# Kernel tuning notes

Hardware: AMD Instinct MI355X
Metric: run time of the kernel (lower is better)

Reference implementation:

```python
import jax, jax.numpy as jnp
import numpy as np

B, S, D, J, NI = 8192, 20, 300, 512, 1000
VG = 2048 + 5 * 6  # vis_dim + 5*6 = guide feature dim


def setup_inputs() -> dict:
    key = jax.random.key(0)
    ks = jax.random.split(key, 11)
    context = jax.random.normal(ks[0], (B, S, D), jnp.float32)
    embedded = jax.random.normal(ks[1], (B, S, D), jnp.float32)
    input_labels = jax.random.randint(ks[2], (B, S), 0, 10000, dtype=jnp.int64)
    # guarantee at least one valid token per row (avoid divide-by-zero renorm)
    input_labels = input_labels.at[:, 0].set(jnp.maximum(input_labels[:, 0], 1))
    guide_input = jax.random.normal(ks[3], (NI, VG), jnp.float32)
    sent_to_image_ann = jax.random.randint(ks[4], (2 * B,), 0, NI, dtype=jnp.int64)
    # parameters (PyTorch Linear: y = x @ W.T + b)
    W_sent = jax.random.normal(ks[5], (J, D), jnp.float32) * 0.02
    b_sent = jnp.zeros((J,), jnp.float32)
    W_emb = jax.random.normal(ks[6], (J, VG), jnp.float32) * 0.02
    b_emb = jnp.zeros((J,), jnp.float32)
    w_fc = jax.random.normal(ks[7], (J,), jnp.float32) * 0.02
    b_fc = jnp.zeros((), jnp.float32)
    return {"context": context, "embedded": embedded, "input_labels": input_labels,
            "guide_input": guide_input, "sent_to_image_ann": sent_to_image_ann,
            "W_sent": W_sent, "b_sent": b_sent, "W_emb": W_emb, "b_emb": b_emb,
            "w_fc": w_fc, "b_fc": b_fc}


def reference(context, embedded, input_labels, guide_input, sent_to_image_ann,
              W_sent, b_sent, W_emb, b_emb, w_fc, b_fc):
    # prefix-valid mask: loop in original breaks at first zero label
    nonzero = (input_labels != 0).astype(jnp.float32)          # (B,S)
    valid = jnp.cumprod(nonzero, axis=1)                        # (B,S)
    # per-sentence guide feature: guide_input[sent_to_image_ann[2*i]]
    fea = guide_input[sent_to_image_ann[::2]]                   # (B,VG)
    # fc_embed(guidance): guidance rows are fea (valid prefix) or 0 (else),
    # so the linear output is fea@W_emb.T+b_emb or just b_emb.
    fea_emb = fea @ W_emb.T + b_emb                             # (B,J)
    guid_emb = valid[:, :, None] * fea_emb[:, None, :] + (1.0 - valid)[:, :, None] * b_emb
    cxt_emb = jnp.einsum('bsd,jd->bsj', context, W_sent) + b_sent
    H = jnp.tanh(cxt_emb + guid_emb)                            # (B,S,J)
    scores = jnp.einsum('bsj,j->bs', H, w_fc) + b_fc            # (B,S)
    attn = jax.nn.softmax(scores, axis=1)
    attn = attn * nonzero
    attn = attn / jnp.sum(attn, axis=1, keepdims=True)
    weighted_cxt = jnp.einsum('bs,bsd->bd', attn, embedded)     # (B,D)
    return weighted_cxt
```

## Files before the change

kernel.cpp:

```cpp
#include <hip/hip_runtime.h>
#include <hip/hip_bf16.h>

#define BB 8192
#define SS 20
#define DD 300
#define JJ 512
#define NII 1000
#define VGG 2078
#define BP1 72

typedef __attribute__((ext_vector_type(8))) short short8v;
typedef __attribute__((ext_vector_type(4))) float float4v;

__device__ __forceinline__ unsigned short bf16u(float x) {
    __hip_bfloat16 h = __float2bfloat16(x);
    return *(unsigned short*)&h;
}

__global__ __launch_bounds__(256) void kc_pad2(const float* __restrict__ W_emb,
                                               const float* __restrict__ guide,
                                               __hip_bfloat16* __restrict__ Web,
                                               __hip_bfloat16* __restrict__ Gb) {
    long idx = (long)blockIdx.x * 256 + threadIdx.x;
    if (idx >= 1512L * 2112) return;
    int r = (int)(idx / 2112), c = (int)(idx % 2112);
    if (r < JJ) {
        float v = (c < VGG) ? W_emb[(long)r * VGG + c] : 0.f;
        Web[(long)r * 2112 + c] = __float2bfloat16(v);
    } else {
        int g = r - JJ;
        float v = (c < VGG) ? guide[(long)g * VGG + c] : 0.f;
        Gb[(long)g * 2112 + c] = __float2bfloat16(v);
    }
}

__global__ __launch_bounds__(256) void kc_prep_wt(const float* __restrict__ W_sent,
                                                  const float* __restrict__ b_sent,
                                                  const float* __restrict__ b_emb,
                                                  __hip_bfloat16* __restrict__ dst) {
    int idx = blockIdx.x * 256 + threadIdx.x;
    if (idx >= 40 * 512) return;
    int kb = idx >> 9, col = idx & 511;
#pragma unroll
    for (int e = 0; e < 8; ++e) {
        int k = kb * 8 + e;
        float v = (k < DD) ? W_sent[(long)col * DD + k]
                : (k == DD) ? b_sent[col]
                : (k == DD + 1) ? b_emb[col] : 0.f;
        dst[(long)idx * 8 + e] = __float2bfloat16(v);
    }
}

__global__ __launch_bounds__(512) void kS_sumwf(const float* __restrict__ w_fc,
                                                float* __restrict__ out) {
    __shared__ float part[8];
    int t = threadIdx.x;
    float v = w_fc[t];
    v += __shfl_xor(v, 1);  v += __shfl_xor(v, 2);  v += __shfl_xor(v, 4);
    v += __shfl_xor(v, 8);  v += __shfl_xor(v, 16); v += __shfl_xor(v, 32);
    if ((t & 63) == 0) part[t >> 6] = v;
    __syncthreads();
    if (t == 0) {
        float s = 0.f;
#pragma unroll
        for (int i = 0; i < 8; ++i) s += part[i];
        out[0] = s;
    }
}

__global__ __launch_bounds__(256) void k0_valid(const int* __restrict__ labels,
                                                float* __restrict__ valid,
                                                float* __restrict__ nonzero) {
    int b = blockIdx.x * blockDim.x + threadIdx.x;
    if (b >= BB) return;
    float v = 1.f;
    for (int s = 0; s < SS; ++s) {
        float nz = (labels[b * SS + s] != 0) ? 1.f : 0.f;
        v *= nz;
        nonzero[b * SS + s] = nz;
        valid[b * SS + s] = v;
    }
}

__global__ __launch_bounds__(256) void k1_femb_mfma(
    const __hip_bfloat16* __restrict__ Gb,
    const __hip_bfloat16* __restrict__ Web,
    const float* __restrict__ b_emb,
    __hip_bfloat16* __restrict__ femb) {
    __shared__ __hip_bfloat16 Al[64 * BP1];
    __shared__ __hip_bfloat16 Bl[64 * BP1];
    const int t = threadIdx.x;
    const int m0 = blockIdx.x * 64;
    const int n0 = blockIdx.y * 64;
    const int lane = t & 63;
    const int w = t >> 6;
    const int wm = w >> 1, wn = w & 1;
    const int li = lane & 15, lq = lane >> 4;

    float4v acc[2][2] = {};

    for (int kt = 0; kt < 33; ++kt) {
        for (int c = t; c < 512; c += 256) {
            int rr = c >> 3, off = (c & 7) * 8;
            int gr = m0 + rr; if (gr > NII - 1) gr = NII - 1;
            *(uint4*)&Al[rr * BP1 + off] =
                *(const uint4*)(Gb + (long)gr * 2112 + kt * 64 + off);
            *(uint4*)&Bl[rr * BP1 + off] =
                *(const uint4*)(Web + (long)(n0 + rr) * 2112 + kt * 64 + off);
        }
        __syncthreads();
#pragma unroll
        for (int ks = 0; ks < 2; ++ks) {
            short8v a[2], b[2];
#pragma unroll
            for (int mt = 0; mt < 2; ++mt)
                a[mt] = *(const short8v*)&Al[(wm * 32 + mt * 16 + li) * BP1 + ks * 32 + lq * 8];
#pragma unroll
            for (int nt = 0; nt < 2; ++nt)
                b[nt] = *(const short8v*)&Bl[(wn * 32 + nt * 16 + li) * BP1 + ks * 32 + lq * 8];
#pragma unroll
            for (int mt = 0; mt < 2; ++mt)
#pragma unroll
                for (int nt = 0; nt < 2; ++nt)
                    acc[mt][nt] = __builtin_amdgcn_mfma_f32_16x16x32_bf16(
                        a[mt], b[nt], acc[mt][nt], 0, 0, 0);
        }
        __syncthreads();
    }
#pragma unroll
    for (int nt = 0; nt < 2; ++nt) {
        int col = n0 + wn * 32 + nt * 16 + li;
        float be = b_emb[col];
#pragma unroll
        for (int mt = 0; mt < 2; ++mt)
#pragma unroll
            for (int reg = 0; reg < 4; ++reg) {
                int row = wm * 32 + mt * 16 + lq * 4 + reg;
                femb[(long)(m0 + row) * JJ + col] = __float2bfloat16(acc[mt][nt][reg] + be);
            }
    }
}

__global__ __launch_bounds__(256)
__attribute__((amdgpu_waves_per_eu(2, 4)))
void k2_scores_mfma(
    const float* __restrict__ context,
    const __hip_bfloat16* __restrict__ Wt,
    const float* __restrict__ w_fc,
    const float* __restrict__ b_fc,
    const float* __restrict__ sumwf,
    const __hip_bfloat16* __restrict__ femb,
    const int* __restrict__ ann,
    const float* __restrict__ valid,
    float* __restrict__ scores) {
    const int t = threadIdx.x;
    const int wid = t >> 6, lane = t & 63;
    const int li = lane & 15, lq = lane >> 4;
    const int m0 = blockIdx.x * 64 + wid * 16;

    const float* crow = context + (long)(m0 + li) * DD;
    const float vA = valid[m0 + li];
    short8v areg[10];
#pragma unroll
    for (int kt = 0; kt < 9; ++kt) {
        const int k0 = kt * 32 + lq * 8;
        float4 u = *(const float4*)(crow + k0);
        float4 v2 = *(const float4*)(crow + k0 + 4);
        short8v a;
        a[0] = (short)bf16u(u.x);  a[1] = (short)bf16u(u.y);
        a[2] = (short)bf16u(u.z);  a[3] = (short)bf16u(u.w);
        a[4] = (short)bf16u(v2.x); a[5] = (short)bf16u(v2.y);
        a[6] = (short)bf16u(v2.z); a[7] = (short)bf16u(v2.w);
        areg[kt] = a;
    }
    {
        short8v a = {0, 0, 0, 0, 0, 0, 0, 0};
        if (lq == 0) {
            float4 u = *(const float4*)(crow + 288);
            float4 v2 = *(const float4*)(crow + 292);
            a[0] = (short)bf16u(u.x);  a[1] = (short)bf16u(u.y);
            a[2] = (short)bf16u(u.z);  a[3] = (short)bf16u(u.w);
            a[4] = (short)bf16u(v2.x); a[5] = (short)bf16u(v2.y);
            a[6] = (short)bf16u(v2.z); a[7] = (short)bf16u(v2.w);
        } else if (lq == 1) {
            float4 u = *(const float4*)(crow + 296);
            a[0] = (short)bf16u(u.x);  a[1] = (short)bf16u(u.y);
            a[2] = (short)bf16u(u.z);  a[3] = (short)bf16u(u.w);
            a[4] = (short)bf16u(1.f);  a[5] = (short)bf16u(1.f - vA);
        }
        areg[9] = a;
    }

    const int mslot = m0 + lq * 4;
    const int b0r = mslot / SS;
    const int b3r = (mslot + 3) / SS;
    const int g0 = ann[2 * b0r];
    const int g1 = ann[2 * b3r];
    float vmc[4]; unsigned selm[4];
#pragma unroll
    for (int reg = 0; reg < 4; ++reg) {
        vmc[reg] = valid[mslot + reg];
        selm[reg] = (((mslot + reg) / SS) != b0r) ? 0xffffffffu : 0u;
    }
    const unsigned short* fp = (const unsigned short*)femb;
    const __hip_bfloat16* pb = Wt + ((long)lq * 512 + li) * 8;

    float sp[4] = {0.f, 0.f, 0.f, 0.f};

    auto loadB = [&](short8v (&buf)[20], int np) {
        const __hip_bfloat16* pn = pb + (long)np * 256;
#pragma unroll
        for (int kt = 0; kt < 10; ++kt) {
            buf[2 * kt]     = *(const short8v*)(pn + (long)kt * 16384);
            buf[2 * kt + 1] = *(const short8v*)(pn + (long)kt * 16384 + 128);
        }
    };
    auto computeB = [&](short8v (&buf)[20], int np) {
        const int colA = np * 32 + li;
        const int colB = colA + 16;
        const unsigned uA = ((unsigned)fp[(long)g1 * JJ + colA] << 16) | fp[(long)g0 * JJ + colA];
        const unsigned uB = ((unsigned)fp[(long)g1 * JJ + colB] << 16) | fp[(long)g0 * JJ + colB];
        const float wfA = w_fc[colA];
        const float wfB = w_fc[colB];
        float4v a0 = {0.f, 0.f, 0.f, 0.f}, a1 = {0.f, 0.f, 0.f, 0.f};
#pragma unroll
        for (int kt = 0; kt < 10; ++kt) {
            a0 = __builtin_amdgcn_mfma_f32_16x16x32_bf16(areg[kt], buf[2 * kt], a0, 0, 0, 0);
            a1 = __builtin_amdgcn_mfma_f32_16x16x32_bf16(areg[kt], buf[2 * kt + 1], a1, 0, 0, 0);
        }
        const unsigned floA = uA << 16, fhiA = uA & 0xffff0000u;
        const unsigned floB = uB << 16, fhiB = uB & 0xffff0000u;
#pragma unroll
        for (int reg = 0; reg < 4; ++reg) {
            const float fvA = __uint_as_float((floA & ~selm[reg]) | (fhiA & selm[reg]));
            const float xA = fmaf(vmc[reg], fvA, a0[reg]);
            const float eA = __expf(xA + xA);
            sp[reg] = fmaf(wfA, __builtin_amdgcn_rcpf(eA + 1.f), sp[reg]);
            const float fvB = __uint_as_float((floB & ~selm[reg]) | (fhiB & selm[reg]));
            const float xB = fmaf(vmc[reg], fvB, a1[reg]);
            const float eB = __expf(xB + xB);
            sp[reg] = fmaf(wfB, __builtin_amdgcn_rcpf(eB + 1.f), sp[reg]);
        }
    };

    short8v bufA[20], bufB[20];
    loadB(bufA, 0);
    for (int nq = 0; nq < 8; ++nq) {
        const int npA = nq * 2;
        loadB(bufB, npA + 1);
        computeB(bufA, npA);
        if (npA + 2 < 16) loadB(bufA, npA + 2);
        computeB(bufB, npA + 1);
    }

    const float base = b_fc[0] + sumwf[0];
#pragma unroll
    for (int reg = 0; reg < 4; ++reg) {
        float v = sp[reg];
        v += __shfl_xor(v, 1); v += __shfl_xor(v, 2);
        v += __shfl_xor(v, 4); v += __shfl_xor(v, 8);
        if (li == 0) scores[mslot + reg] = base - 2.f * v;
    }
}

__global__ __launch_bounds__(256) void k3_out(const float* __restrict__ scores,
                                              const float* __restrict__ nonzero,
                                              const float* __restrict__ embedded,
                                              float* __restrict__ out) {
    __shared__ float wgt[3][SS];
    const int b0 = blockIdx.x * 3;
    const int t = threadIdx.x;
    if (t < 3) {
        int b = b0 + t;
        if (b < BB) {
            float sc[SS], nz[SS];
            float mx = -1e30f;
            for (int s = 0; s < SS; ++s) {
                sc[s] = scores[b * SS + s];
                nz[s] = nonzero[b * SS + s];
                mx = fmaxf(mx, sc[s]);
            }
            float den = 0.f, e[SS];
            for (int s = 0; s < SS; ++s) { e[s] = nz[s] * __expf(sc[s] - mx); den += e[s]; }
            float inv = 1.f / den;
            for (int s = 0; s < SS; ++s) wgt[t][s] = e[s] * inv;
        }
    }
    __syncthreads();
    if (t < 225) {
        int r = t / 75, q = t - r * 75;
        int b = b0 + r;
        if (b < BB) {
            float4 a; a.x = a.y = a.z = a.w = 0.f;
#pragma unroll
            for (int s = 0; s < SS; ++s) {
                float4 e = *(const float4*)(embedded + ((long)b * SS + s) * DD + q * 4);
                float ww = wgt[r][s];
                a.x += ww * e.x; a.y += ww * e.y; a.z += ww * e.z; a.w += ww * e.w;
            }
            *(float4*)(out + (long)b * DD + q * 4) = a;
        }
    }
}

extern "C" void kernel_launch(void* const* d_in, const int* in_sizes, int n_in,
                              void* d_out, int out_size, void* d_ws, size_t ws_size,
                              hipStream_t stream) {
    const float* context  = (const float*)d_in[0];
    const float* embedded = (const float*)d_in[1];
    const int*   labels   = (const int*)d_in[2];
    const float* guide    = (const float*)d_in[3];
    const int*   ann      = (const int*)d_in[4];
    const float* W_sent   = (const float*)d_in[5];
    const float* b_sent   = (const float*)d_in[6];
    const float* W_emb    = (const float*)d_in[7];
    const float* b_emb    = (const float*)d_in[8];
    const float* w_fc     = (const float*)d_in[9];
    const float* b_fc     = (const float*)d_in[10];
    float* out = (float*)d_out;

    char* w = (char*)d_ws;
    __hip_bfloat16* femb = (__hip_bfloat16*)(w);
    float* valid         = (float*)(w + 1048576);
    float* nonzero       = (float*)(w + 1703936);
    float* scores        = (float*)(w + 2359296);
    __hip_bfloat16* Wt   = (__hip_bfloat16*)(w + 3014656);
    __hip_bfloat16* Web  = (__hip_bfloat16*)(w + 3342336);
    __hip_bfloat16* Gb   = (__hip_bfloat16*)(w + 5505024);
    float* sums          = (float*)(w + 9729024);

    hipLaunchKernelGGL(kc_prep_wt, dim3((40 * 512 + 255) / 256), dim3(256), 0, stream,
                       W_sent, b_sent, b_emb, Wt);
    hipLaunchKernelGGL(kc_pad2, dim3((int)((1512L * 2112 + 255) / 256)), dim3(256), 0, stream,
                       W_emb, guide, Web, Gb);
    hipLaunchKernelGGL(kS_sumwf, dim3(1), dim3(512), 0, stream, w_fc, sums);
    hipLaunchKernelGGL(k0_valid, dim3(BB / 256), dim3(256), 0, stream,
                       labels, valid, nonzero);
    hipLaunchKernelGGL(k1_femb_mfma, dim3(16, JJ / 64), dim3(256), 0, stream,
                       Gb, Web, b_emb, femb);
    hipLaunchKernelGGL(k2_scores_mfma, dim3((BB * SS) / 64), dim3(256), 0, stream,
                       context, Wt, w_fc, b_fc, sums, femb, ann, valid, scores);
    hipLaunchKernelGGL(k3_out, dim3((BB + 2) / 3), dim3(256), 0, stream,
                       scores, nonzero, embedded, out);
}
```

Measured before the change: 238.5 us.

## Process two 16-row M tiles per wave in scores kernel to reuse B fragments

Each wave in k2_scores_mfma now computes 32 rows (two 16-row MFMA tiles) instead of 16. Every loaded W_sent fragment therefore feeds two MFMAs, which halves global/L2 traffic for the weight operand per row, and the grid is halved to match. The occupancy hint is tightened to 2 waves/EU and the outer loop is fully unrolled. The cost is much higher register pressure, with doubled A registers and accumulators, plus lower occupancy, which could cause spills or less latency hiding.

```diff
diff --git a/kernel.cpp b/kernel.cpp
--- a/kernel.cpp
+++ b/kernel.cpp
@@ -142,7 +142,7 @@
 }
 
 __global__ __launch_bounds__(256)
-__attribute__((amdgpu_waves_per_eu(2, 4)))
+__attribute__((amdgpu_waves_per_eu(2, 2)))
 void k2_scores_mfma(
     const float* __restrict__ context,
     const __hip_bfloat16* __restrict__ Wt,
@@ -156,24 +156,25 @@
     const int t = threadIdx.x;
     const int wid = t >> 6, lane = t & 63;
     const int li = lane & 15, lq = lane >> 4;
-    const int m0 = blockIdx.x * 64 + wid * 16;
-
-    const float* crow = context + (long)(m0 + li) * DD;
-    const float vA = valid[m0 + li];
-    short8v areg[10];
-#pragma unroll
-    for (int kt = 0; kt < 9; ++kt) {
-        const int k0 = kt * 32 + lq * 8;
-        float4 u = *(const float4*)(crow + k0);
-        float4 v2 = *(const float4*)(crow + k0 + 4);
-        short8v a;
-        a[0] = (short)bf16u(u.x);  a[1] = (short)bf16u(u.y);
-        a[2] = (short)bf16u(u.z);  a[3] = (short)bf16u(u.w);
-        a[4] = (short)bf16u(v2.x); a[5] = (short)bf16u(v2.y);
-        a[6] = (short)bf16u(v2.z); a[7] = (short)bf16u(v2.w);
-        areg[kt] = a;
-    }
-    {
+    const int m0 = blockIdx.x * 128 + wid * 32;
+
+    short8v areg0[10], areg1[10];
+#pragma unroll
+    for (int mh = 0; mh < 2; ++mh) {
+        const float* crow = context + (long)(m0 + mh * 16 + li) * DD;
+        const float vA = valid[m0 + mh * 16 + li];
+#pragma unroll
+        for (int kt = 0; kt < 9; ++kt) {
+            const int k0 = kt * 32 + lq * 8;
+            float4 u = *(const float4*)(crow + k0);
+            float4 v2 = *(const float4*)(crow + k0 + 4);
+            short8v a;
+            a[0] = (short)bf16u(u.x);  a[1] = (short)bf16u(u.y);
+            a[2] = (short)bf16u(u.z);  a[3] = (short)bf16u(u.w);
+            a[4] = (short)bf16u(v2.x); a[5] = (short)bf16u(v2.y);
+            a[6] = (short)bf16u(v2.z); a[7] = (short)bf16u(v2.w);
+            if (mh == 0) areg0[kt] = a; else areg1[kt] = a;
+        }
         short8v a = {0, 0, 0, 0, 0, 0, 0, 0};
         if (lq == 0) {
             float4 u = *(const float4*)(crow + 288);
@@ -188,24 +189,27 @@
             a[2] = (short)bf16u(u.z);  a[3] = (short)bf16u(u.w);
             a[4] = (short)bf16u(1.f);  a[5] = (short)bf16u(1.f - vA);
         }
-        areg[9] = a;
-    }
-
-    const int mslot = m0 + lq * 4;
-    const int b0r = mslot / SS;
-    const int b3r = (mslot + 3) / SS;
-    const int g0 = ann[2 * b0r];
-    const int g1 = ann[2 * b3r];
-    float vmc[4]; unsigned selm[4];
-#pragma unroll
-    for (int reg = 0; reg < 4; ++reg) {
-        vmc[reg] = valid[mslot + reg];
-        selm[reg] = (((mslot + reg) / SS) != b0r) ? 0xffffffffu : 0u;
+        if (mh == 0) areg0[9] = a; else areg1[9] = a;
+    }
+
+    int g0_[2], g1_[2];
+    float vmc[2][4]; unsigned selm[2][4];
+#pragma unroll
+    for (int mh = 0; mh < 2; ++mh) {
+        const int mslot = m0 + mh * 16 + lq * 4;
+        const int b0r = mslot / SS;
+        g0_[mh] = ann[2 * b0r];
+        g1_[mh] = ann[2 * ((mslot + 3) / SS)];
+#pragma unroll
+        for (int reg = 0; reg < 4; ++reg) {
+            vmc[mh][reg] = valid[mslot + reg];
+            selm[mh][reg] = (((mslot + reg) / SS) != b0r) ? 0xffffffffu : 0u;
+        }
     }
     const unsigned short* fp = (const unsigned short*)femb;
     const __hip_bfloat16* pb = Wt + ((long)lq * 512 + li) * 8;
 
-    float sp[4] = {0.f, 0.f, 0.f, 0.f};
+    float sp[2][4] = {};
 
     auto loadB = [&](short8v (&buf)[20], int np) {
         const __hip_bfloat16* pn = pb + (long)np * 256;
@@ -218,33 +222,47 @@
     auto computeB = [&](short8v (&buf)[20], int np) {
         const int colA = np * 32 + li;
         const int colB = colA + 16;
-        const unsigned uA = ((unsigned)fp[(long)g1 * JJ + colA] << 16) | fp[(long)g0 * JJ + colA];
-        const unsigned uB = ((unsigned)fp[(long)g1 * JJ + colB] << 16) | fp[(long)g0 * JJ + colB];
         const float wfA = w_fc[colA];
         const float wfB = w_fc[colB];
-        float4v a0 = {0.f, 0.f, 0.f, 0.f}, a1 = {0.f, 0.f, 0.f, 0.f};
+        unsigned uA[2], uB[2];
+#pragma unroll
+        for (int mh = 0; mh < 2; ++mh) {
+            uA[mh] = ((unsigned)fp[(long)g1_[mh] * JJ + colA] << 16) | fp[(long)g0_[mh] * JJ + colA];
+            uB[mh] = ((unsigned)fp[(long)g1_[mh] * JJ + colB] << 16) | fp[(long)g0_[mh] * JJ + colB];
+        }
+        float4v a00 = {0.f, 0.f, 0.f, 0.f}, a01 = {0.f, 0.f, 0.f, 0.f};
+        float4v a10 = {0.f, 0.f, 0.f, 0.f}, a11 = {0.f, 0.f, 0.f, 0.f};
 #pragma unroll
         for (int kt = 0; kt < 10; ++kt) {
-            a0 = __builtin_amdgcn_mfma_f32_16x16x32_bf16(areg[kt], buf[2 * kt], a0, 0, 0, 0);
-            a1 = __builtin_amdgcn_mfma_f32_16x16x32_bf16(areg[kt], buf[2 * kt + 1], a1, 0, 0, 0);
-        }
-        const unsigned floA = uA << 16, fhiA = uA & 0xffff0000u;
-        const unsigned floB = uB << 16, fhiB = uB & 0xffff0000u;
-#pragma unroll
-        for (int reg = 0; reg < 4; ++reg) {
-            const float fvA = __uint_as_float((floA & ~selm[reg]) | (fhiA & selm[reg]));
-            const float xA = fmaf(vmc[reg], fvA, a0[reg]);
-            const float eA = __expf(xA + xA);
-            sp[reg] = fmaf(wfA, __builtin_amdgcn_rcpf(eA + 1.f), sp[reg]);
-            const float fvB = __uint_as_float((floB & ~selm[reg]) | (fhiB & selm[reg]));
-            const float xB = fmaf(vmc[reg], fvB, a1[reg]);
-            const float eB = __expf(xB + xB);
-            sp[reg] = fmaf(wfB, __builtin_amdgcn_rcpf(eB + 1.f), sp[reg]);
+            const short8v b0 = buf[2 * kt], b1 = buf[2 * kt + 1];
+            a00 = __builtin_amdgcn_mfma_f32_16x16x32_bf16(areg0[kt], b0, a00, 0, 0, 0);
+            a10 = __builtin_amdgcn_mfma_f32_16x16x32_bf16(areg1[kt], b0, a10, 0, 0, 0);
+            a01 = __builtin_amdgcn_mfma_f32_16x16x32_bf16(areg0[kt], b1, a01, 0, 0, 0);
+            a11 = __builtin_amdgcn_mfma_f32_16x16x32_bf16(areg1[kt], b1, a11, 0, 0, 0);
+        }
+#pragma unroll
+        for (int mh = 0; mh < 2; ++mh) {
+            const unsigned floA = uA[mh] << 16, fhiA = uA[mh] & 0xffff0000u;
+            const unsigned floB = uB[mh] << 16, fhiB = uB[mh] & 0xffff0000u;
+#pragma unroll
+            for (int reg = 0; reg < 4; ++reg) {
+                const float fvA = __uint_as_float((floA & ~selm[mh][reg]) | (fhiA & selm[mh][reg]));
+                const float aA = (mh == 0) ? a00[reg] : a10[reg];
+                const float xA = fmaf(vmc[mh][reg], fvA, aA);
+                const float eA = __expf(xA + xA);
+                sp[mh][reg] = fmaf(wfA, __builtin_amdgcn_rcpf(eA + 1.f), sp[mh][reg]);
+                const float fvB = __uint_as_float((floB & ~selm[mh][reg]) | (fhiB & selm[mh][reg]));
+                const float aB = (mh == 0) ? a01[reg] : a11[reg];
+                const float xB = fmaf(vmc[mh][reg], fvB, aB);
+                const float eB = __expf(xB + xB);
+                sp[mh][reg] = fmaf(wfB, __builtin_amdgcn_rcpf(eB + 1.f), sp[mh][reg]);
+            }
         }
     };
 
     short8v bufA[20], bufB[20];
     loadB(bufA, 0);
+#pragma unroll
     for (int nq = 0; nq < 8; ++nq) {
         const int npA = nq * 2;
         loadB(bufB, npA + 1);
@@ -255,12 +273,14 @@
 
     const float base = b_fc[0] + sumwf[0];
 #pragma unroll
-    for (int reg = 0; reg < 4; ++reg) {
-        float v = sp[reg];
-        v += __shfl_xor(v, 1); v += __shfl_xor(v, 2);
-        v += __shfl_xor(v, 4); v += __shfl_xor(v, 8);
-        if (li == 0) scores[mslot + reg] = base - 2.f * v;
-    }
+    for (int mh = 0; mh < 2; ++mh)
+#pragma unroll
+        for (int reg = 0; reg < 4; ++reg) {
+            float v = sp[mh][reg];
+            v += __shfl_xor(v, 1); v += __shfl_xor(v, 2);
+            v += __shfl_xor(v, 4); v += __shfl_xor(v, 8);
+            if (li == 0) scores[m0 + mh * 16 + lq * 4 + reg] = base - 2.f * v;
+        }
 }
 
 __global__ __launch_bounds__(256) void k3_out(const float* __restrict__ scores,
@@ -338,7 +358,7 @@
                        labels, valid, nonzero);
     hipLaunchKernelGGL(k1_femb_mfma, dim3(16, JJ / 64), dim3(256), 0, stream,
                        Gb, Web, b_emb, femb);
-    hipLaunchKernelGGL(k2_scores_mfma, dim3((BB * SS) / 64), dim3(256), 0, stream,
+    hipLaunchKernelGGL(k2_scores_mfma, dim3((BB * SS) / 128), dim3(256), 0, stream,
                        context, Wt, w_fc, b_fc, sums, femb, ann, valid, scores);
     hipLaunchKernelGGL(k3_out, dim3((BB + 2) / 3), dim3(256), 0, stream,
                        scores, nonzero, embedded, out);
```

After: 701.2 us. +194.1%, slower.
